# Kernel optimization log

Hardware: AMD Instinct MI355X
Metric: run time of the kernel (lower is better)

Reference implementation:

```python
import jax, jax.numpy as jnp
import numpy as np
import math

C = 768; H = 12; B = 2; TX = 2048; TC = 2048

def setup_inputs() -> dict:
    key = jax.random.key(0)
    ks = jax.random.split(key, 20)
    w = lambda k, s: jax.random.normal(k, s, dtype=jnp.float32) * 0.02
    inp = {
        "x": jax.random.normal(ks[0], (B, TX, C), dtype=jnp.float32),
        "context": jax.random.normal(ks[1], (B, TC, C), dtype=jnp.float32),
        "ln1_g": jnp.ones((C,), jnp.float32), "ln1_b": jnp.zeros((C,), jnp.float32),
        "ln2_g": jnp.ones((C,), jnp.float32), "ln2_b": jnp.zeros((C,), jnp.float32),
        "ln3_g": jnp.ones((C,), jnp.float32), "ln3_b": jnp.zeros((C,), jnp.float32),
        "sa_wq": w(ks[2], (C, C)), "sa_bq": jnp.zeros((C,), jnp.float32),
        "sa_wk": w(ks[3], (C, C)), "sa_bk": jnp.zeros((C,), jnp.float32),
        "sa_wv": w(ks[4], (C, C)), "sa_bv": jnp.zeros((C,), jnp.float32),
        "sa_wo": w(ks[5], (C, C)), "sa_bo": jnp.zeros((C,), jnp.float32),
        "xa_wq": w(ks[6], (C, C)), "xa_bq": jnp.zeros((C,), jnp.float32),
        "xa_wk": w(ks[7], (C, C)), "xa_bk": jnp.zeros((C,), jnp.float32),
        "xa_wv": w(ks[8], (C, C)), "xa_bv": jnp.zeros((C,), jnp.float32),
        "xa_wo": w(ks[9], (C, C)), "xa_bo": jnp.zeros((C,), jnp.float32),
        "mlp_w1": w(ks[10], (C, 4 * C)), "mlp_b1": jnp.zeros((4 * C,), jnp.float32),
        "mlp_w2": w(ks[11], (4 * C, C)), "mlp_b2": jnp.zeros((C,), jnp.float32),
        "n_head": H,
    }
    return inp

def _layernorm(x, g, b, eps=1e-5):
    mu = jnp.mean(x, axis=-1, keepdims=True)
    var = jnp.mean(jnp.square(x - mu), axis=-1, keepdims=True)
    return (x - mu) * jax.lax.rsqrt(var + eps) * g + b

def _attn(xq, xkv, wq, bq, wk, bk, wv, bv, wo, bo, n_head):
    Bq, Tq, Cm = xq.shape
    Tk = xkv.shape[1]
    dh = Cm // n_head
    q = (xq @ wq + bq).reshape(Bq, Tq, n_head, dh)
    k = (xkv @ wk + bk).reshape(Bq, Tk, n_head, dh)
    v = (xkv @ wv + bv).reshape(Bq, Tk, n_head, dh)
    att = jnp.einsum('bqhd,bkhd->bhqk', q, k) * (1.0 / math.sqrt(dh))
    att = jax.nn.softmax(att, axis=-1)
    y = jnp.einsum('bhqk,bkhd->bqhd', att, v).reshape(Bq, Tq, Cm)
    return y @ wo + bo

def reference(x, context, ln1_g, ln1_b, ln2_g, ln2_b, ln3_g, ln3_b,
              sa_wq, sa_bq, sa_wk, sa_bk, sa_wv, sa_bv, sa_wo, sa_bo,
              xa_wq, xa_bq, xa_wk, xa_bk, xa_wv, xa_bv, xa_wo, xa_bo,
              mlp_w1, mlp_b1, mlp_w2, mlp_b2, n_head):
    # pre-LN residual self-attention
    x = x + _attn(_layernorm(x, ln1_g, ln1_b), _layernorm(x, ln1_g, ln1_b),
                  sa_wq, sa_bq, sa_wk, sa_bk, sa_wv, sa_bv, sa_wo, sa_bo, n_head)
    # pre-LN residual cross-attention (context not normalized, matching source)
    x = x + _attn(_layernorm(x, ln2_g, ln2_b), context,
                  xa_wq, xa_bq, xa_wk, xa_bk, xa_wv, xa_bv, xa_wo, xa_bo, n_head)
    # pre-LN residual MLP with exact (erf) GELU, as torch.nn.GELU default
    h = _layernorm(x, ln3_g, ln3_b)
    x = x + (jax.nn.gelu(h @ mlp_w1 + mlp_b1, approximate=False) @ mlp_w2 + mlp_b2)
    return (x, context)
```

## Files before the change

kernel.cpp:

```cpp
#include <hip/hip_runtime.h>
#include <hip/hip_bf16.h>
#include <math.h>

#define CDIM 768
#define HDIM 3072
#define NROWS 4096
#define TSEQ 2048
#define NHEAD 12
#define KVSPLIT 2
#define KVLEN (TSEQ / KVSPLIT)

typedef unsigned short u16;
typedef unsigned int   u32;
typedef __attribute__((ext_vector_type(8))) short short8;
typedef __attribute__((ext_vector_type(4))) float f32x4;

#define QSCALE 0.18033688011112042f

static __device__ __forceinline__ u16 f2bf(float f) {
    u32 x = __float_as_uint(f);
    x += 0x7fffu + ((x >> 16) & 1u);
    return (u16)(x >> 16);
}
static __device__ __forceinline__ u32 cvt_pk_bf16(float lo, float hi) {
    u32 r;
    asm("v_cvt_pk_bf16_f32 %0, %1, %2" : "=v"(r) : "v"(lo), "v"(hi));
    return r;
}

#define GLL16(g, l)                                                            \
    __builtin_amdgcn_global_load_lds(                                          \
        (const __attribute__((address_space(1))) void*)(g),                    \
        (__attribute__((address_space(3))) void*)(l), 16, 0, 0)

__launch_bounds__(256)
__global__ void wtrans(const float* __restrict__ w, u16* __restrict__ wt,
                       int K, int N) {
    __shared__ float t[32][33];
    const int n0 = blockIdx.x * 32, k0 = blockIdx.y * 32;
    const int tx = threadIdx.x & 31, ty = threadIdx.x >> 5;
#pragma unroll
    for (int i = ty; i < 32; i += 8)
        t[i][tx] = w[(size_t)(k0 + i) * N + n0 + tx];
    __syncthreads();
#pragma unroll
    for (int i = ty; i < 32; i += 8)
        wt[(size_t)(n0 + i) * K + k0 + tx] = f2bf(t[tx][i]);
}

__launch_bounds__(256)
__global__ void cvt_copy(const float* __restrict__ in, u16* __restrict__ out,
                         int n4) {
    int i = blockIdx.x * 256 + threadIdx.x;
    if (i >= n4) return;
    float4 v = ((const float4*)in)[i];
    ushort4 o;
    o.x = f2bf(v.x); o.y = f2bf(v.y); o.z = f2bf(v.z); o.w = f2bf(v.w);
    ((ushort4*)out)[i] = o;
}

__launch_bounds__(256)
__global__ void ln_kernel(const float* __restrict__ x, const float* __restrict__ g,
                          const float* __restrict__ bta, u16* __restrict__ out) {
    const int row = blockIdx.x, tid = threadIdx.x;
    const float* xr = x + (size_t)row * CDIM;
    float v0 = xr[tid], v1 = xr[tid + 256], v2 = xr[tid + 512];
    __shared__ float red[8];
    float s = v0 + v1 + v2;
#pragma unroll
    for (int m = 1; m < 64; m <<= 1) s += __shfl_xor(s, m);
    if ((tid & 63) == 0) red[tid >> 6] = s;
    __syncthreads();
    const float mu = (red[0] + red[1] + red[2] + red[3]) * (1.f / CDIM);
    const float d0 = v0 - mu, d1 = v1 - mu, d2 = v2 - mu;
    float q = d0 * d0 + d1 * d1 + d2 * d2;
#pragma unroll
    for (int m = 1; m < 64; m <<= 1) q += __shfl_xor(q, m);
    if ((tid & 63) == 0) red[4 + (tid >> 6)] = q;
    __syncthreads();
    const float var = (red[4] + red[5] + red[6] + red[7]) * (1.f / CDIM);
    const float rstd = rsqrtf(var + 1e-5f);
    u16* orow = out + (size_t)row * CDIM;
    orow[tid]       = f2bf(d0 * rstd * g[tid]       + bta[tid]);
    orow[tid + 256] = f2bf(d1 * rstd * g[tid + 256] + bta[tid + 256]);
    orow[tid + 512] = f2bf(d2 * rstd * g[tid + 512] + bta[tid + 512]);
}

struct GemmArgs {
    const u16* A[3];
    const u16* BT[3];
    const float* bias[3];
    const float* res[3];
    void* out[3];
    float alpha[3];
    int M, N, K;
};

template <int EPI, int BM>
__launch_bounds__(256)
__global__ void gemm_bt(GemmArgs ga) {
    constexpr int MF = BM / 32;
    __shared__ u16 Abuf[BM * 32];
    __shared__ u16 Bbuf[128 * 32];
    const int z = blockIdx.z;
    const u16* __restrict__ A  = ga.A[z];
    const u16* __restrict__ BT = ga.BT[z];
    const float* __restrict__ bias = ga.bias[z];
    const float* __restrict__ res  = ga.res[z];
    void* outv = ga.out[z];
    const float alpha = ga.alpha[z];
    const int N = ga.N, K = ga.K;

    const int tid = threadIdx.x;
    const int lane = tid & 63, w = tid >> 6;
    const int m0 = blockIdx.x * BM, n0 = blockIdx.y * 128;
    const int wr = (w >> 1) * (BM / 2), wc = (w & 1) * 64;
    const int lr = lane & 15, lc = lane >> 4;

    const int srowA = w * (BM / 4) + (lane >> 2);
    const int srowB = w * 32 + (lane >> 2);
    const int scol = (lane & 3) * 8;
    const u16* Ag = A + (size_t)(m0 + srowA) * K + scol;
    const u16* Bg = BT + (size_t)(n0 + srowB) * K + scol;
    char* Ab = (char*)Abuf + w * (BM * 16);
    char* Bb = (char*)Bbuf + w * 2048;

    f32x4 acc[MF][4];
#pragma unroll
    for (int m = 0; m < MF; ++m)
#pragma unroll
        for (int n = 0; n < 4; ++n) acc[m][n] = (f32x4){0.f, 0.f, 0.f, 0.f};

    const int nk = K >> 5;
    for (int kt = 0; kt < nk; ++kt) {
        const int ko = kt * 32;
        GLL16(Ag + ko, Ab);
        if constexpr (BM == 128) GLL16(Ag + 16 * K + ko, Ab + 1024);
        GLL16(Bg + ko,          Bb);
        GLL16(Bg + 16 * K + ko, Bb + 1024);
        __syncthreads();
        short8 af[MF], bfv[4];
#pragma unroll
        for (int m = 0; m < MF; ++m)
            af[m] = *(const short8*)((const char*)Abuf +
                                     (size_t)(wr + m * 16 + lr) * 64 + lc * 16);
#pragma unroll
        for (int n = 0; n < 4; ++n)
            bfv[n] = *(const short8*)((const char*)Bbuf +
                                      (size_t)(wc + n * 16 + lr) * 64 + lc * 16);
#pragma unroll
        for (int m = 0; m < MF; ++m)
#pragma unroll
            for (int n = 0; n < 4; ++n)
                acc[m][n] = __builtin_amdgcn_mfma_f32_16x16x32_bf16(
                    af[m], bfv[n], acc[m][n], 0, 0, 0);
        __syncthreads();
    }

#pragma unroll
    for (int n = 0; n < 4; ++n) {
        const int gc = n0 + wc + n * 16 + lr;
        const float bs = bias[gc];
#pragma unroll
        for (int m = 0; m < MF; ++m) {
            const int gr = m0 + wr + m * 16 + lc * 4;
#pragma unroll
            for (int r = 0; r < 4; ++r) {
                float v = (acc[m][n][r] + bs) * alpha;
                const size_t idx = (size_t)(gr + r) * N + gc;
                if constexpr (EPI == 0) {
                    ((u16*)outv)[idx] = f2bf(v);
                } else if constexpr (EPI == 1) {
                    ((float*)outv)[idx] = res[idx] + v;
                } else {
                    float gel = 0.5f * v * (1.0f + erff(v * 0.70710678118654752f));
                    ((u16*)outv)[idx] = f2bf(gel);
                }
            }
        }
    }
}

__launch_bounds__(256)
__global__ void attn_split(const u16* __restrict__ Qb, const u16* __restrict__ Kb,
                           const u16* __restrict__ Vb, float* __restrict__ Opart,
                           float2* __restrict__ ml) {
    __shared__ u16 Klds[64 * 72];
    __shared__ u16 Vt[64 * 72];
    const int tid = threadIdx.x;
    const int lane = tid & 63, w = tid >> 6;
    const int lr = lane & 15, lc = lane >> 4;
    const int b = blockIdx.y / NHEAD, h = blockIdx.y % NHEAD;
    const int z = blockIdx.z;
    const size_t qrow0 = (size_t)b * TSEQ + blockIdx.x * 64 + w * 16;
    const size_t krow0 = (size_t)b * TSEQ + (size_t)z * KVLEN;
    const int hc = h * 64;

    short8 qf0, qf1;
    {
        const u16* qp = Qb + (qrow0 + lr) * CDIM + hc + lc * 8;
        qf0 = *(const short8*)qp;
        qf1 = *(const short8*)(qp + 32);
    }
    f32x4 oacc[4];
#pragma unroll
    for (int r = 0; r < 4; ++r) oacc[r] = (f32x4){0.f, 0.f, 0.f, 0.f};
    float mrow = -3e38f, lrow = 0.f;

    const int stg_r = tid >> 2, stg_s = tid & 3;
    const u16* kg = Kb + (krow0 + stg_r) * CDIM + hc + stg_s * 16;
    const u16* vg = Vb + (krow0 + stg_r) * CDIM + hc + stg_s * 16;
    uint4 ka0 = *(const uint4*)kg, ka1 = *(const uint4*)(kg + 8);
    uint4 va0 = *(const uint4*)vg, va1 = *(const uint4*)(vg + 8);
    const int sig = ((stg_r >> 5) << 5) + (((stg_r >> 2) & 3) << 3) +
                    (((stg_r >> 4) & 1) << 2) + (stg_r & 3);
    char* vdst = (char*)Vt + ((2 * sig) ^ (stg_s << 5)) +
                 (size_t)(stg_s * 16) * 144;

    for (int kt = 0; kt < KVLEN / 64; ++kt) {
        __syncthreads();
        {
            *(uint4*)&Klds[stg_r * 72 + stg_s * 16]     = ka0;
            *(uint4*)&Klds[stg_r * 72 + stg_s * 16 + 8] = ka1;
            u16 tmp[16];
            *(uint4*)(tmp)     = va0;
            *(uint4*)(tmp + 8) = va1;
#pragma unroll
            for (int j = 0; j < 16; ++j)
                *(u16*)(vdst + (size_t)j * 144) = tmp[j];
        }
        if (kt < KVLEN / 64 - 1) {
            kg += 64 * CDIM; vg += 64 * CDIM;
            ka0 = *(const uint4*)kg; ka1 = *(const uint4*)(kg + 8);
            va0 = *(const uint4*)vg; va1 = *(const uint4*)(vg + 8);
        }
        __syncthreads();

        f32x4 sf[4];
#pragma unroll
        for (int fn = 0; fn < 4; ++fn) {
            const u16* kr = &Klds[(lr + fn * 16) * 72 + lc * 8];
            short8 kb0 = *(const short8*)kr;
            short8 kb1 = *(const short8*)(kr + 32);
            f32x4 t = (f32x4){0.f, 0.f, 0.f, 0.f};
            t = __builtin_amdgcn_mfma_f32_16x16x32_bf16(kb0, qf0, t, 0, 0, 0);
            t = __builtin_amdgcn_mfma_f32_16x16x32_bf16(kb1, qf1, t, 0, 0, 0);
            sf[fn] = t;
        }

        float pm;
        {
            float a0 = fmaxf(fmaxf(sf[0][0], sf[0][1]), fmaxf(sf[0][2], sf[0][3]));
            float a1 = fmaxf(fmaxf(sf[1][0], sf[1][1]), fmaxf(sf[1][2], sf[1][3]));
            float a2 = fmaxf(fmaxf(sf[2][0], sf[2][1]), fmaxf(sf[2][2], sf[2][3]));
            float a3 = fmaxf(fmaxf(sf[3][0], sf[3][1]), fmaxf(sf[3][2], sf[3][3]));
            pm = fmaxf(fmaxf(a0, a1), fmaxf(a2, a3));
            pm = fmaxf(pm, __shfl_xor(pm, 16));
            pm = fmaxf(pm, __shfl_xor(pm, 32));
        }
        const float mn = fmaxf(mrow, pm);
        const float corr = exp2f(mrow - mn);
        mrow = mn;
        float rs;
        {
#pragma unroll
            for (int fn = 0; fn < 4; ++fn)
#pragma unroll
                for (int r = 0; r < 4; ++r) sf[fn][r] = exp2f(sf[fn][r] - mn);
            float s0 = (sf[0][0] + sf[0][1]) + (sf[0][2] + sf[0][3]);
            float s1 = (sf[1][0] + sf[1][1]) + (sf[1][2] + sf[1][3]);
            float s2 = (sf[2][0] + sf[2][1]) + (sf[2][2] + sf[2][3]);
            float s3 = (sf[3][0] + sf[3][1]) + (sf[3][2] + sf[3][3]);
            rs = (s0 + s1) + (s2 + s3);
            rs += __shfl_xor(rs, 16);
            rs += __shfl_xor(rs, 32);
        }
        lrow = lrow * corr + rs;
#pragma unroll
        for (int fd = 0; fd < 4; ++fd)
#pragma unroll
            for (int r = 0; r < 4; ++r) oacc[fd][r] *= corr;

        int4 pw0, pw1;
        pw0.x = cvt_pk_bf16(sf[0][0], sf[0][1]);
        pw0.y = cvt_pk_bf16(sf[0][2], sf[0][3]);
        pw0.z = cvt_pk_bf16(sf[1][0], sf[1][1]);
        pw0.w = cvt_pk_bf16(sf[1][2], sf[1][3]);
        pw1.x = cvt_pk_bf16(sf[2][0], sf[2][1]);
        pw1.y = cvt_pk_bf16(sf[2][2], sf[2][3]);
        pw1.z = cvt_pk_bf16(sf[3][0], sf[3][1]);
        pw1.w = cvt_pk_bf16(sf[3][2], sf[3][3]);
        short8 pb0 = *(short8*)&pw0;
        short8 pb1 = *(short8*)&pw1;

#pragma unroll
        for (int fd = 0; fd < 4; ++fd) {
            const char* vtb = (const char*)Vt + (size_t)(lr + fd * 16) * 144;
            short8 vb0 = *(const short8*)(vtb + ((lc * 16) ^ (fd * 32)));
            short8 vb1 = *(const short8*)(vtb + ((lc * 16 + 64) ^ (fd * 32)));
            oacc[fd] = __builtin_amdgcn_mfma_f32_16x16x32_bf16(vb0, pb0, oacc[fd], 0, 0, 0);
            oacc[fd] = __builtin_amdgcn_mfma_f32_16x16x32_bf16(vb1, pb1, oacc[fd], 0, 0, 0);
        }
    }

    float* obase = Opart + (size_t)z * NROWS * CDIM + (qrow0 + lr) * CDIM + hc + lc * 4;
#pragma unroll
    for (int fd = 0; fd < 4; ++fd) {
        float4 o = {oacc[fd][0], oacc[fd][1], oacc[fd][2], oacc[fd][3]};
        *(float4*)(obase + fd * 16) = o;
    }
    if (lc == 0)
        ml[((size_t)z * NROWS + qrow0 + lr) * NHEAD + h] = (float2){mrow, lrow};
}

__launch_bounds__(256)
__global__ void attn_merge(const float* __restrict__ P0, const float* __restrict__ P1,
                           const float2* __restrict__ ml, u16* __restrict__ out) {
    const int i4 = blockIdx.x * 256 + threadIdx.x;
    const size_t base = (size_t)i4 * 4;
    const int row = (int)(base / CDIM);
    const int head = (int)(base - (size_t)row * CDIM) >> 6;
    const float2 a = ml[(size_t)row * NHEAD + head];
    const float2 c = ml[((size_t)NROWS + row) * NHEAD + head];
    const float M = fmaxf(a.x, c.x);
    const float e0 = exp2f(a.x - M), e1 = exp2f(c.x - M);
    const float rden = 1.f / (a.y * e0 + c.y * e1);
    const float4 p0 = *(const float4*)(P0 + base);
    const float4 p1 = *(const float4*)(P1 + base);
    ushort4 o;
    o.x = f2bf((p0.x * e0 + p1.x * e1) * rden);
    o.y = f2bf((p0.y * e0 + p1.y * e1) * rden);
    o.z = f2bf((p0.z * e0 + p1.z * e1) * rden);
    o.w = f2bf((p0.w * e0 + p1.w * e1) * rden);
    *(ushort4*)(out + base) = o;
}

extern "C" void kernel_launch(void* const* d_in, const int* in_sizes, int n_in,
                              void* d_out, int out_size, void* d_ws, size_t ws_size,
                              hipStream_t stream) {
    const float* x     = (const float*)d_in[0];
    const float* ctx   = (const float*)d_in[1];
    const float* ln1g  = (const float*)d_in[2];
    const float* ln1b  = (const float*)d_in[3];
    const float* ln2g  = (const float*)d_in[4];
    const float* ln2b  = (const float*)d_in[5];
    const float* ln3g  = (const float*)d_in[6];
    const float* ln3b  = (const float*)d_in[7];
    const float* sa_wq = (const float*)d_in[8];
    const float* sa_bq = (const float*)d_in[9];
    const float* sa_wk = (const float*)d_in[10];
    const float* sa_bk = (const float*)d_in[11];
    const float* sa_wv = (const float*)d_in[12];
    const float* sa_bv = (const float*)d_in[13];
    const float* sa_wo = (const float*)d_in[14];
    const float* sa_bo = (const float*)d_in[15];
    const float* xa_wq = (const float*)d_in[16];
    const float* xa_bq = (const float*)d_in[17];
    const float* xa_wk = (const float*)d_in[18];
    const float* xa_bk = (const float*)d_in[19];
    const float* xa_wv = (const float*)d_in[20];
    const float* xa_bv = (const float*)d_in[21];
    const float* xa_wo = (const float*)d_in[22];
    const float* xa_bo = (const float*)d_in[23];
    const float* m_w1  = (const float*)d_in[24];
    const float* m_b1  = (const float*)d_in[25];
    const float* m_w2  = (const float*)d_in[26];
    const float* m_b2  = (const float*)d_in[27];

    float* out_x   = (float*)d_out;
    float* out_ctx = out_x + (size_t)NROWS * CDIM;
    float* Opart   = (float*)d_out;

    const size_t SZ_ACT  = (size_t)NROWS * CDIM * 2;
    const size_t SZ_WBIG = (size_t)HDIM * CDIM * 2;
    const size_t SZ_R    = (size_t)NROWS * CDIM * 4;
    const size_t NEEDED  = 5 * SZ_ACT + SZ_R + SZ_WBIG;
    if (ws_size < NEEDED) return;

    char* ws = (char*)d_ws;
    u16* qb    = (u16*)(ws);
    u16* kb    = (u16*)(ws + 1 * SZ_ACT);
    u16* vb    = (u16*)(ws + 2 * SZ_ACT);
    u16* ctxb  = (u16*)(ws + 3 * SZ_ACT);
    u16* hb    = qb;
    u16* lnbuf = (u16*)(ws + 4 * SZ_ACT);
    u16* attB  = lnbuf;
    float* R   = (float*)(ws + 5 * SZ_ACT);
    u16* Wq    = (u16*)(ws + 5 * SZ_ACT + SZ_R);
    u16* Wk    = Wq + (size_t)CDIM * CDIM;
    u16* Wv    = Wk + (size_t)CDIM * CDIM;
    float2* ml = (float2*)Wq;

    const dim3 tb(256);
    GemmArgs ga;

    cvt_copy<<<dim3(3072), tb, 0, stream>>>(ctx, ctxb, NROWS * CDIM / 4);

    ln_kernel<<<dim3(NROWS), tb, 0, stream>>>(x, ln1g, ln1b, lnbuf);
    wtrans<<<dim3(24, 24), tb, 0, stream>>>(sa_wq, Wq, 768, 768);
    wtrans<<<dim3(24, 24), tb, 0, stream>>>(sa_wk, Wk, 768, 768);
    wtrans<<<dim3(24, 24), tb, 0, stream>>>(sa_wv, Wv, 768, 768);
    ga = GemmArgs{};
    ga.A[0] = lnbuf; ga.BT[0] = Wq; ga.bias[0] = sa_bq; ga.out[0] = qb; ga.alpha[0] = QSCALE;
    ga.A[1] = lnbuf; ga.BT[1] = Wk; ga.bias[1] = sa_bk; ga.out[1] = kb; ga.alpha[1] = 1.f;
    ga.A[2] = lnbuf; ga.BT[2] = Wv; ga.bias[2] = sa_bv; ga.out[2] = vb; ga.alpha[2] = 1.f;
    ga.M = 4096; ga.N = 768; ga.K = 768;
    gemm_bt<0, 128><<<dim3(32, 6, 3), tb, 0, stream>>>(ga);
    attn_split<<<dim3(32, 24, KVSPLIT), tb, 0, stream>>>(qb, kb, vb, Opart, ml);
    attn_merge<<<dim3(NROWS * CDIM / 1024), tb, 0, stream>>>(
        Opart, Opart + (size_t)NROWS * CDIM, ml, attB);
    wtrans<<<dim3(24, 24), tb, 0, stream>>>(sa_wo, Wq, 768, 768);
    ga = GemmArgs{};
    ga.A[0] = attB; ga.BT[0] = Wq; ga.bias[0] = sa_bo; ga.res[0] = x; ga.out[0] = R; ga.alpha[0] = 1.f;
    ga.M = 4096; ga.N = 768; ga.K = 768;
    gemm_bt<1, 64><<<dim3(64, 6, 1), tb, 0, stream>>>(ga);

    ln_kernel<<<dim3(NROWS), tb, 0, stream>>>(R, ln2g, ln2b, lnbuf);
    wtrans<<<dim3(24, 24), tb, 0, stream>>>(xa_wq, Wq, 768, 768);
    wtrans<<<dim3(24, 24), tb, 0, stream>>>(xa_wk, Wk, 768, 768);
    wtrans<<<dim3(24, 24), tb, 0, stream>>>(xa_wv, Wv, 768, 768);
    ga = GemmArgs{};
    ga.A[0] = lnbuf; ga.BT[0] = Wq; ga.bias[0] = xa_bq; ga.out[0] = qb; ga.alpha[0] = QSCALE;
    ga.A[1] = ctxb;  ga.BT[1] = Wk; ga.bias[1] = xa_bk; ga.out[1] = kb; ga.alpha[1] = 1.f;
    ga.A[2] = ctxb;  ga.BT[2] = Wv; ga.bias[2] = xa_bv; ga.out[2] = vb; ga.alpha[2] = 1.f;
    ga.M = 4096; ga.N = 768; ga.K = 768;
    gemm_bt<0, 128><<<dim3(32, 6, 3), tb, 0, stream>>>(ga);
    attn_split<<<dim3(32, 24, KVSPLIT), tb, 0, stream>>>(qb, kb, vb, Opart, ml);
    attn_merge<<<dim3(NROWS * CDIM / 1024), tb, 0, stream>>>(
        Opart, Opart + (size_t)NROWS * CDIM, ml, attB);
    hipMemcpyAsync(out_ctx, ctx, (size_t)NROWS * CDIM * 4,
                   hipMemcpyDeviceToDevice, stream);
    wtrans<<<dim3(24, 24), tb, 0, stream>>>(xa_wo, Wq, 768, 768);
    ga = GemmArgs{};
    ga.A[0] = attB; ga.BT[0] = Wq; ga.bias[0] = xa_bo; ga.res[0] = R; ga.out[0] = R; ga.alpha[0] = 1.f;
    ga.M = 4096; ga.N = 768; ga.K = 768;
    gemm_bt<1, 64><<<dim3(64, 6, 1), tb, 0, stream>>>(ga);

    ln_kernel<<<dim3(NROWS), tb, 0, stream>>>(R, ln3g, ln3b, lnbuf);
    wtrans<<<dim3(96, 24), tb, 0, stream>>>(m_w1, Wq, 768, 3072);
    ga = GemmArgs{};
    ga.A[0] = lnbuf; ga.BT[0] = Wq; ga.bias[0] = m_b1; ga.out[0] = hb; ga.alpha[0] = 1.f;
    ga.M = 4096; ga.N = 3072; ga.K = 768;
    gemm_bt<2, 128><<<dim3(32, 24, 1), tb, 0, stream>>>(ga);
    wtrans<<<dim3(24, 96), tb, 0, stream>>>(m_w2, Wq, 3072, 768);
    ga = GemmArgs{};
    ga.A[0] = hb; ga.BT[0] = Wq; ga.bias[0] = m_b2; ga.res[0] = R; ga.out[0] = out_x; ga.alpha[0] = 1.f;
    ga.M = 4096; ga.N = 768; ga.K = 3072;
    gemm_bt<1, 64><<<dim3(64, 6, 1), tb, 0, stream>>>(ga);

    (void)in_sizes; (void)n_in; (void)out_size;
}
```

Baseline: 392.4 us.

## Raise KV split to 4, store bf16 partials, add lazy rescale and smaller GEMM tiles

The attention KV split goes from 2 to 4 to put more blocks in flight, and partial outputs are stored as bf16 instead of fp32, with a generalized merge kernel. The online-softmax rescale of the accumulator is skipped when no lane's running max increases. The three per-layer weight transposes are batched into one launch, and the N=768 residual GEMMs use 64x64 tiles to double their grid. The goal is better occupancy and less launch and memory traffic, at the cost of bf16 rounding on the partials and more merge reads.

```diff
diff --git a/kernel.cpp b/kernel.cpp
--- a/kernel.cpp
+++ b/kernel.cpp
@@ -7,7 +7,7 @@
 #define NROWS 4096
 #define TSEQ 2048
 #define NHEAD 12
-#define KVSPLIT 2
+#define KVSPLIT 4
 #define KVLEN (TSEQ / KVSPLIT)
 
 typedef unsigned short u16;
@@ -21,6 +21,9 @@
     u32 x = __float_as_uint(f);
     x += 0x7fffu + ((x >> 16) & 1u);
     return (u16)(x >> 16);
+}
+static __device__ __forceinline__ float bf2f(u16 x) {
+    return __uint_as_float((u32)x << 16);
 }
 static __device__ __forceinline__ u32 cvt_pk_bf16(float lo, float hi) {
     u32 r;
@@ -46,6 +49,23 @@
 #pragma unroll
     for (int i = ty; i < 32; i += 8)
         wt[(size_t)(n0 + i) * K + k0 + tx] = f2bf(t[tx][i]);
+}
+
+struct WT3 { const float* w[3]; u16* wt[3]; };
+__launch_bounds__(256)
+__global__ void wtrans3(WT3 a) {
+    __shared__ float t[32][33];
+    const float* __restrict__ w = a.w[blockIdx.z];
+    u16* __restrict__ wt = a.wt[blockIdx.z];
+    const int n0 = blockIdx.x * 32, k0 = blockIdx.y * 32;
+    const int tx = threadIdx.x & 31, ty = threadIdx.x >> 5;
+#pragma unroll
+    for (int i = ty; i < 32; i += 8)
+        t[i][tx] = w[(size_t)(k0 + i) * CDIM + n0 + tx];
+    __syncthreads();
+#pragma unroll
+    for (int i = ty; i < 32; i += 8)
+        wt[(size_t)(n0 + i) * CDIM + k0 + tx] = f2bf(t[tx][i]);
 }
 
 __launch_bounds__(256)
@@ -96,12 +116,12 @@
     int M, N, K;
 };
 
-template <int EPI, int BM>
+template <int EPI, int BM, int BN = 128>
 __launch_bounds__(256)
 __global__ void gemm_bt(GemmArgs ga) {
-    constexpr int MF = BM / 32;
+    constexpr int MF = BM / 32, NF = BN / 32;
     __shared__ u16 Abuf[BM * 32];
-    __shared__ u16 Bbuf[128 * 32];
+    __shared__ u16 Bbuf[BN * 32];
     const int z = blockIdx.z;
     const u16* __restrict__ A  = ga.A[z];
     const u16* __restrict__ BT = ga.BT[z];
@@ -113,52 +133,52 @@
 
     const int tid = threadIdx.x;
     const int lane = tid & 63, w = tid >> 6;
-    const int m0 = blockIdx.x * BM, n0 = blockIdx.y * 128;
-    const int wr = (w >> 1) * (BM / 2), wc = (w & 1) * 64;
+    const int m0 = blockIdx.x * BM, n0 = blockIdx.y * BN;
+    const int wr = (w >> 1) * (BM / 2), wc = (w & 1) * (BN / 2);
     const int lr = lane & 15, lc = lane >> 4;
 
-    const int srowA = w * (BM / 4) + (lane >> 2);
-    const int srowB = w * 32 + (lane >> 2);
+    const int srowA = (BM == 128) ? (w * 32 + (lane >> 2)) : (tid >> 2);
+    const int srowB = (BN == 128) ? (w * 32 + (lane >> 2)) : (tid >> 2);
     const int scol = (lane & 3) * 8;
     const u16* Ag = A + (size_t)(m0 + srowA) * K + scol;
     const u16* Bg = BT + (size_t)(n0 + srowB) * K + scol;
-    char* Ab = (char*)Abuf + w * (BM * 16);
-    char* Bb = (char*)Bbuf + w * 2048;
-
-    f32x4 acc[MF][4];
+    char* Ab = (char*)Abuf + w * (BM == 128 ? 2048 : 1024);
+    char* Bb = (char*)Bbuf + w * (BN == 128 ? 2048 : 1024);
+
+    f32x4 acc[MF][NF];
 #pragma unroll
     for (int m = 0; m < MF; ++m)
 #pragma unroll
-        for (int n = 0; n < 4; ++n) acc[m][n] = (f32x4){0.f, 0.f, 0.f, 0.f};
+        for (int n = 0; n < NF; ++n) acc[m][n] = (f32x4){0.f, 0.f, 0.f, 0.f};
 
     const int nk = K >> 5;
     for (int kt = 0; kt < nk; ++kt) {
         const int ko = kt * 32;
         GLL16(Ag + ko, Ab);
         if constexpr (BM == 128) GLL16(Ag + 16 * K + ko, Ab + 1024);
-        GLL16(Bg + ko,          Bb);
-        GLL16(Bg + 16 * K + ko, Bb + 1024);
+        GLL16(Bg + ko, Bb);
+        if constexpr (BN == 128) GLL16(Bg + 16 * K + ko, Bb + 1024);
         __syncthreads();
-        short8 af[MF], bfv[4];
+        short8 af[MF], bfv[NF];
 #pragma unroll
         for (int m = 0; m < MF; ++m)
             af[m] = *(const short8*)((const char*)Abuf +
                                      (size_t)(wr + m * 16 + lr) * 64 + lc * 16);
 #pragma unroll
-        for (int n = 0; n < 4; ++n)
+        for (int n = 0; n < NF; ++n)
             bfv[n] = *(const short8*)((const char*)Bbuf +
                                       (size_t)(wc + n * 16 + lr) * 64 + lc * 16);
 #pragma unroll
         for (int m = 0; m < MF; ++m)
 #pragma unroll
-            for (int n = 0; n < 4; ++n)
+            for (int n = 0; n < NF; ++n)
                 acc[m][n] = __builtin_amdgcn_mfma_f32_16x16x32_bf16(
                     af[m], bfv[n], acc[m][n], 0, 0, 0);
         __syncthreads();
     }
 
 #pragma unroll
-    for (int n = 0; n < 4; ++n) {
+    for (int n = 0; n < NF; ++n) {
         const int gc = n0 + wc + n * 16 + lr;
         const float bs = bias[gc];
 #pragma unroll
@@ -183,7 +203,7 @@
 
 __launch_bounds__(256)
 __global__ void attn_split(const u16* __restrict__ Qb, const u16* __restrict__ Kb,
-                           const u16* __restrict__ Vb, float* __restrict__ Opart,
+                           const u16* __restrict__ Vb, u16* __restrict__ Opart,
                            float2* __restrict__ ml) {
     __shared__ u16 Klds[64 * 72];
     __shared__ u16 Vt[64 * 72];
@@ -258,15 +278,22 @@
             pm = fmaxf(pm, __shfl_xor(pm, 16));
             pm = fmaxf(pm, __shfl_xor(pm, 32));
         }
-        const float mn = fmaxf(mrow, pm);
-        const float corr = exp2f(mrow - mn);
-        mrow = mn;
+        if (!__all(pm <= mrow)) {
+            const float mn = fmaxf(mrow, pm);
+            const float corr = exp2f(mrow - mn);
+            mrow = mn;
+            lrow *= corr;
+#pragma unroll
+            for (int fd = 0; fd < 4; ++fd)
+#pragma unroll
+                for (int r = 0; r < 4; ++r) oacc[fd][r] *= corr;
+        }
         float rs;
         {
 #pragma unroll
             for (int fn = 0; fn < 4; ++fn)
 #pragma unroll
-                for (int r = 0; r < 4; ++r) sf[fn][r] = exp2f(sf[fn][r] - mn);
+                for (int r = 0; r < 4; ++r) sf[fn][r] = exp2f(sf[fn][r] - mrow);
             float s0 = (sf[0][0] + sf[0][1]) + (sf[0][2] + sf[0][3]);
             float s1 = (sf[1][0] + sf[1][1]) + (sf[1][2] + sf[1][3]);
             float s2 = (sf[2][0] + sf[2][1]) + (sf[2][2] + sf[2][3]);
@@ -275,11 +302,7 @@
             rs += __shfl_xor(rs, 16);
             rs += __shfl_xor(rs, 32);
         }
-        lrow = lrow * corr + rs;
-#pragma unroll
-        for (int fd = 0; fd < 4; ++fd)
-#pragma unroll
-            for (int r = 0; r < 4; ++r) oacc[fd][r] *= corr;
+        lrow += rs;
 
         int4 pw0, pw1;
         pw0.x = cvt_pk_bf16(sf[0][0], sf[0][1]);
@@ -303,35 +326,51 @@
         }
     }
 
-    float* obase = Opart + (size_t)z * NROWS * CDIM + (qrow0 + lr) * CDIM + hc + lc * 4;
+    u16* obase = Opart + (size_t)z * NROWS * CDIM + (qrow0 + lr) * CDIM + hc + lc * 4;
 #pragma unroll
     for (int fd = 0; fd < 4; ++fd) {
-        float4 o = {oacc[fd][0], oacc[fd][1], oacc[fd][2], oacc[fd][3]};
-        *(float4*)(obase + fd * 16) = o;
+        ushort4 o;
+        o.x = f2bf(oacc[fd][0]); o.y = f2bf(oacc[fd][1]);
+        o.z = f2bf(oacc[fd][2]); o.w = f2bf(oacc[fd][3]);
+        *(ushort4*)(obase + fd * 16) = o;
     }
     if (lc == 0)
         ml[((size_t)z * NROWS + qrow0 + lr) * NHEAD + h] = (float2){mrow, lrow};
 }
 
 __launch_bounds__(256)
-__global__ void attn_merge(const float* __restrict__ P0, const float* __restrict__ P1,
-                           const float2* __restrict__ ml, u16* __restrict__ out) {
+__global__ void attn_merge4(const u16* __restrict__ P, const float2* __restrict__ ml,
+                            u16* __restrict__ out) {
     const int i4 = blockIdx.x * 256 + threadIdx.x;
     const size_t base = (size_t)i4 * 4;
     const int row = (int)(base / CDIM);
     const int head = (int)(base - (size_t)row * CDIM) >> 6;
-    const float2 a = ml[(size_t)row * NHEAD + head];
-    const float2 c = ml[((size_t)NROWS + row) * NHEAD + head];
-    const float M = fmaxf(a.x, c.x);
-    const float e0 = exp2f(a.x - M), e1 = exp2f(c.x - M);
-    const float rden = 1.f / (a.y * e0 + c.y * e1);
-    const float4 p0 = *(const float4*)(P0 + base);
-    const float4 p1 = *(const float4*)(P1 + base);
+    float2 a[KVSPLIT];
+    float M = -3e38f;
+#pragma unroll
+    for (int z = 0; z < KVSPLIT; ++z) {
+        a[z] = ml[((size_t)z * NROWS + row) * NHEAD + head];
+        M = fmaxf(M, a[z].x);
+    }
+    float den = 0.f, e[KVSPLIT];
+#pragma unroll
+    for (int z = 0; z < KVSPLIT; ++z) {
+        e[z] = exp2f(a[z].x - M);
+        den += a[z].y * e[z];
+    }
+    const float rden = 1.f / den;
+    float o0 = 0.f, o1 = 0.f, o2 = 0.f, o3 = 0.f;
+#pragma unroll
+    for (int z = 0; z < KVSPLIT; ++z) {
+        ushort4 p = *(const ushort4*)(P + (size_t)z * NROWS * CDIM + base);
+        o0 += bf2f(p.x) * e[z];
+        o1 += bf2f(p.y) * e[z];
+        o2 += bf2f(p.z) * e[z];
+        o3 += bf2f(p.w) * e[z];
+    }
     ushort4 o;
-    o.x = f2bf((p0.x * e0 + p1.x * e1) * rden);
-    o.y = f2bf((p0.y * e0 + p1.y * e1) * rden);
-    o.z = f2bf((p0.z * e0 + p1.z * e1) * rden);
-    o.w = f2bf((p0.w * e0 + p1.w * e1) * rden);
+    o.x = f2bf(o0 * rden); o.y = f2bf(o1 * rden);
+    o.z = f2bf(o2 * rden); o.w = f2bf(o3 * rden);
     *(ushort4*)(out + base) = o;
 }
 
@@ -369,7 +408,7 @@
 
     float* out_x   = (float*)d_out;
     float* out_ctx = out_x + (size_t)NROWS * CDIM;
-    float* Opart   = (float*)d_out;
+    u16* Opart = (u16*)d_out;
 
     const size_t SZ_ACT  = (size_t)NROWS * CDIM * 2;
     const size_t SZ_WBIG = (size_t)HDIM * CDIM * 2;
@@ -393,13 +432,14 @@
 
     const dim3 tb(256);
     GemmArgs ga;
+    WT3 wg;
 
     cvt_copy<<<dim3(3072), tb, 0, stream>>>(ctx, ctxb, NROWS * CDIM / 4);
 
     ln_kernel<<<dim3(NROWS), tb, 0, stream>>>(x, ln1g, ln1b, lnbuf);
-    wtrans<<<dim3(24, 24), tb, 0, stream>>>(sa_wq, Wq, 768, 768);
-    wtrans<<<dim3(24, 24), tb, 0, stream>>>(sa_wk, Wk, 768, 768);
-    wtrans<<<dim3(24, 24), tb, 0, stream>>>(sa_wv, Wv, 768, 768);
+    wg.w[0] = sa_wq; wg.w[1] = sa_wk; wg.w[2] = sa_wv;
+    wg.wt[0] = Wq;   wg.wt[1] = Wk;   wg.wt[2] = Wv;
+    wtrans3<<<dim3(24, 24, 3), tb, 0, stream>>>(wg);
     ga = GemmArgs{};
     ga.A[0] = lnbuf; ga.BT[0] = Wq; ga.bias[0] = sa_bq; ga.out[0] = qb; ga.alpha[0] = QSCALE;
     ga.A[1] = lnbuf; ga.BT[1] = Wk; ga.bias[1] = sa_bk; ga.out[1] = kb; ga.alpha[1] = 1.f;
@@ -407,18 +447,17 @@
     ga.M = 4096; ga.N = 768; ga.K = 768;
     gemm_bt<0, 128><<<dim3(32, 6, 3), tb, 0, stream>>>(ga);
     attn_split<<<dim3(32, 24, KVSPLIT), tb, 0, stream>>>(qb, kb, vb, Opart, ml);
-    attn_merge<<<dim3(NROWS * CDIM / 1024), tb, 0, stream>>>(
-        Opart, Opart + (size_t)NROWS * CDIM, ml, attB);
+    attn_merge4<<<dim3(NROWS * CDIM / 1024), tb, 0, stream>>>(Opart, ml, attB);
     wtrans<<<dim3(24, 24), tb, 0, stream>>>(sa_wo, Wq, 768, 768);
     ga = GemmArgs{};
     ga.A[0] = attB; ga.BT[0] = Wq; ga.bias[0] = sa_bo; ga.res[0] = x; ga.out[0] = R; ga.alpha[0] = 1.f;
     ga.M = 4096; ga.N = 768; ga.K = 768;
-    gemm_bt<1, 64><<<dim3(64, 6, 1), tb, 0, stream>>>(ga);
+    gemm_bt<1, 64, 64><<<dim3(64, 12, 1), tb, 0, stream>>>(ga);
 
     ln_kernel<<<dim3(NROWS), tb, 0, stream>>>(R, ln2g, ln2b, lnbuf);
-    wtrans<<<dim3(24, 24), tb, 0, stream>>>(xa_wq, Wq, 768, 768);
-    wtrans<<<dim3(24, 24), tb, 0, stream>>>(xa_wk, Wk, 768, 768);
-    wtrans<<<dim3(24, 24), tb, 0, stream>>>(xa_wv, Wv, 768, 768);
+    wg.w[0] = xa_wq; wg.w[1] = xa_wk; wg.w[2] = xa_wv;
+    wg.wt[0] = Wq;   wg.wt[1] = Wk;   wg.wt[2] = Wv;
+    wtrans3<<<dim3(24, 24, 3), tb, 0, stream>>>(wg);
     ga = GemmArgs{};
     ga.A[0] = lnbuf; ga.BT[0] = Wq; ga.bias[0] = xa_bq; ga.out[0] = qb; ga.alpha[0] = QSCALE;
     ga.A[1] = ctxb;  ga.BT[1] = Wk; ga.bias[1] = xa_bk; ga.out[1] = kb; ga.alpha[1] = 1.f;
@@ -426,15 +465,14 @@
     ga.M = 4096; ga.N = 768; ga.K = 768;
     gemm_bt<0, 128><<<dim3(32, 6, 3), tb, 0, stream>>>(ga);
     attn_split<<<dim3(32, 24, KVSPLIT), tb, 0, stream>>>(qb, kb, vb, Opart, ml);
-    attn_merge<<<dim3(NROWS * CDIM / 1024), tb, 0, stream>>>(
-        Opart, Opart + (size_t)NROWS * CDIM, ml, attB);
+    attn_merge4<<<dim3(NROWS * CDIM / 1024), tb, 0, stream>>>(Opart, ml, attB);
     hipMemcpyAsync(out_ctx, ctx, (size_t)NROWS * CDIM * 4,
                    hipMemcpyDeviceToDevice, stream);
     wtrans<<<dim3(24, 24), tb, 0, stream>>>(xa_wo, Wq, 768, 768);
     ga = GemmArgs{};
     ga.A[0] = attB; ga.BT[0] = Wq; ga.bias[0] = xa_bo; ga.res[0] = R; ga.out[0] = R; ga.alpha[0] = 1.f;
     ga.M = 4096; ga.N = 768; ga.K = 768;
-    gemm_bt<1, 64><<<dim3(64, 6, 1), tb, 0, stream>>>(ga);
+    gemm_bt<1, 64, 64><<<dim3(64, 12, 1), tb, 0, stream>>>(ga);
 
     ln_kernel<<<dim3(NROWS), tb, 0, stream>>>(R, ln3g, ln3b, lnbuf);
     wtrans<<<dim3(96, 24), tb, 0, stream>>>(m_w1, Wq, 768, 3072);
@@ -446,7 +484,7 @@
     ga = GemmArgs{};
     ga.A[0] = hb; ga.BT[0] = Wq; ga.bias[0] = m_b2; ga.res[0] = R; ga.out[0] = out_x; ga.alpha[0] = 1.f;
     ga.M = 4096; ga.N = 768; ga.K = 3072;
-    gemm_bt<1, 64><<<dim3(64, 6, 1), tb, 0, stream>>>(ga);
+    gemm_bt<1, 64, 64><<<dim3(64, 12, 1), tb, 0, stream>>>(ga);
 
     (void)in_sizes; (void)n_in; (void)out_size;
 }
```

Result: faster. 362.4 us (-7.7%).
